# Performance work log

Hardware: AMD Instinct MI355X
Metric: run time of the kernel (lower is better)

The kernel has to match this reference:

```python
import jax, jax.numpy as jnp
import numpy as np

B, S, D = 4, 1024, 1024
H = 16
HD = D // H  # 64
NPOS = 64


def setup_inputs() -> dict:
    key = jax.random.key(0)
    ks = jax.random.split(key, 12)
    f = lambda k, shape, s=0.02: jax.random.normal(k, shape, dtype=jnp.float32) * s
    return {
        "q": jax.random.normal(ks[0], (B, S, D), dtype=jnp.float32),
        "k": jax.random.normal(ks[1], (B, S, D), dtype=jnp.float32),
        "v": jax.random.normal(ks[2], (B, S, D), dtype=jnp.float32),
        "Wq_w": f(ks[3], (D, D)), "Wq_b": f(ks[4], (D,)),
        "Wk_w": f(ks[5], (D, D)), "Wk_b": f(ks[6], (D,)),
        "Wv_w": f(ks[7], (D, D)), "Wv_b": f(ks[8], (D,)),
        "Wo_w": f(ks[9], (D, D)), "Wo_b": f(ks[10], (D,)),
        "pos_emb": f(ks[11], (HD, NPOS)),  # torch param is [1,1,head_dim,npos_max]
    }


def _proj(x, w, b):
    # nn.Linear: x @ w.T + b, then split heads -> [B, H, S, HD]
    y = jnp.einsum("bsd,ed->bse", x, w) + b
    bsz, s, _ = y.shape
    return y.reshape(bsz, s, H, HD).transpose(0, 2, 1, 3)


def reference(q, k, v, Wq_w, Wq_b, Wk_w, Wk_b, Wv_w, Wv_b, Wo_w, Wo_b, pos_emb):
    Q = _proj(q, Wq_w, Wq_b)
    K = _proj(k, Wk_w, Wk_b)
    V = _proj(v, Wv_w, Wv_b)

    scale = 1.0 / np.sqrt(HD).astype(np.float32)
    logits = jnp.einsum("bhqd,bhkd->bhqk", Q, K) * scale  # [B,H,S,S]

    # CoPE: sigmoid gates -> reverse cumsum -> interpolated position-logit gather
    gates = jax.nn.sigmoid(logits)
    pos = jnp.flip(jnp.cumsum(jnp.flip(gates, axis=-1), axis=-1), axis=-1)
    pos = jnp.minimum(pos, NPOS - 1)
    pos_floor = jnp.floor(pos)
    pos_ceil = jnp.ceil(pos)
    logits_int = jnp.einsum("bhqd,dn->bhqn", Q, pos_emb)  # [B,H,S,NPOS]
    lc = jnp.take_along_axis(logits_int, pos_ceil.astype(jnp.int32), axis=-1)
    lf = jnp.take_along_axis(logits_int, pos_floor.astype(jnp.int32), axis=-1)
    w = pos - pos_floor
    logits = logits + lc * w + lf * (1.0 - w)

    score = jax.nn.softmax(logits, axis=-1)
    out = jnp.einsum("bhqk,bhkd->bhqd", score, V)
    out = out.transpose(0, 2, 1, 3).reshape(q.shape[0], q.shape[1], D)
    return jnp.einsum("bsd,ed->bse", out, Wo_w) + Wo_b
```

## Files before the change

### kernel.cpp

```cpp
#include <hip/hip_runtime.h>
#include <hip/hip_bf16.h>

typedef __attribute__((ext_vector_type(8))) short short8;
typedef __attribute__((ext_vector_type(4))) float f32x4;
typedef unsigned short us;

#define MFMA16(a,b,c) __builtin_amdgcn_mfma_f32_16x16x32_bf16((a),(b),(c),0,0,0)
#define LOG2E 1.4426950408889634f

static __device__ __forceinline__ us bf16r(float x){
  unsigned u = __builtin_bit_cast(unsigned, x);
  u = u + 0x7fffu + ((u >> 16) & 1u);
  return (us)(u >> 16);
}
static __device__ __forceinline__ unsigned cvtpk(float a, float b){
  unsigned r; asm("v_cvt_pk_bf16_f32 %0, %1, %2" : "=v"(r) : "v"(a), "v"(b)); return r;
}
static __device__ __forceinline__ short8 cvt8(float4 a, float4 b){
  uint4 u; u.x = cvtpk(a.x, a.y); u.y = cvtpk(a.z, a.w);
  u.z = cvtpk(b.x, b.y); u.w = cvtpk(b.z, b.w);
  return __builtin_bit_cast(short8, u);
}
static __device__ __forceinline__ float b2f(us h){
  return __builtin_bit_cast(float, (unsigned)h << 16);
}
static __device__ __forceinline__ float exp2fast(float x){
  float r; asm("v_exp_f32 %0, %1" : "=v"(r) : "v"(x)); return r;
}
static __device__ __forceinline__ float rcpfast(float x){
  float r; asm("v_rcp_f32 %0, %1" : "=v"(r) : "v"(x)); return r;
}
static __device__ __forceinline__ float fractfast(float x){
  float r; asm("v_fract_f32 %0, %1" : "=v"(r) : "v"(x)); return r;
}
template<int CTRL, int RMASK>
static __device__ __forceinline__ float dpp_add(float x){
  int t = __builtin_amdgcn_update_dpp(0, __builtin_bit_cast(int, x), CTRL, RMASK, 0xf, false);
  return x + __builtin_bit_cast(float, t);
}
static __device__ __forceinline__ float wave_iscan(float x){
  x = dpp_add<0x111, 0xf>(x);
  x = dpp_add<0x112, 0xf>(x);
  x = dpp_add<0x114, 0xf>(x);
  x = dpp_add<0x118, 0xf>(x);
  x = dpp_add<0x142, 0xa>(x);
  x = dpp_add<0x143, 0xc>(x);
  return x;
}
static __device__ __forceinline__ float lane63(float x){
  return __builtin_bit_cast(float, __builtin_amdgcn_readlane(__builtin_bit_cast(int, x), 63));
}

__global__ __launch_bounds__(256)
void transpose_pe(const float* __restrict__ pe, us* __restrict__ peT){
  const int t = threadIdx.x;
  const int n = t & 63, dq = t >> 6;
#pragma unroll
  for (int j = 0; j < 16; ++j){
    const int d = dq * 16 + j;
    peT[n * 64 + d] = bf16r(pe[d * 64 + n] * LOG2E);
  }
}

__global__ __launch_bounds__(256)
void transpose_v(const us* __restrict__ Vb, us* __restrict__ VT){
  __shared__ __align__(16) us tile[64 * 72];
  const int t = threadIdx.x;
  const int stile = blockIdx.x & 15;
  const int bh = blockIdx.x >> 4;
  const int b = bh >> 4, h = bh & 15;
  const int s0 = stile << 6;
#pragma unroll
  for (int c = 0; c < 2; ++c){
    const int idx = t + (c << 8);
    const int sr = idx >> 3, cw = idx & 7;
    *(short8*)&tile[sr * 72 + cw * 8] =
        *(const short8*)(Vb + ((size_t)(b * 1024 + s0 + sr)) * 1024 + h * 64 + cw * 8);
  }
  __syncthreads();
#pragma unroll
  for (int c = 0; c < 2; ++c){
    const int idx = t + (c << 8);
    const int dr = idx >> 3, sw = idx & 7;
    short8 o;
#pragma unroll
    for (int j = 0; j < 8; ++j) o[j] = (short)tile[(sw * 8 + j) * 72 + dr];
    *(short8*)(VT + ((size_t)(bh * 64 + dr)) * 1024 + s0 + sw * 8) = o;
  }
}

template<bool A_BF16, bool OUT_BF16>
__global__ __launch_bounds__(256)
void gemm3(const void* __restrict__ Av0, const void* __restrict__ Av1, const void* __restrict__ Av2,
           const float* __restrict__ W0, const float* __restrict__ W1, const float* __restrict__ W2,
           const float* __restrict__ bp0, const float* __restrict__ bp1, const float* __restrict__ bp2,
           void* __restrict__ O0, void* __restrict__ O1, void* __restrict__ O2){
  __shared__ __align__(16) us Al[128 * 64];
  __shared__ __align__(16) us Bl[128 * 64];
  const int sel = blockIdx.y;
  const void* Av   = sel == 0 ? Av0 : (sel == 1 ? Av1 : Av2);
  const float* Wm  = sel == 0 ? W0  : (sel == 1 ? W1  : W2);
  const float* bias = sel == 0 ? bp0 : (sel == 1 ? bp1 : bp2);
  void* Ov         = sel == 0 ? O0  : (sel == 1 ? O1  : O2);
  const int tid = threadIdx.x;
  const int bm = blockIdx.x & 31, bn = blockIdx.x >> 5;
  const int m0 = bm << 7, n0 = bn << 7;
  const int w = tid >> 6, l = tid & 63;
  const int lr = l & 15, lg = l >> 4;
  const int wm = (w & 1) << 6, wn = (w >> 1) << 6;
  int srow[4], scol[4], sdst[4];
#pragma unroll
  for (int c = 0; c < 4; ++c){
    const int idx = tid + (c << 8);
    const int r = idx >> 3, cw = idx & 7;
    srow[c] = r; scol[c] = cw << 3;
    sdst[c] = r * 64 + ((cw << 3) ^ ((r & 7) << 3));
  }
  const int swz = (lr & 7) << 3;
  f32x4 acc[4][4];
#pragma unroll
  for (int i = 0; i < 4; ++i)
#pragma unroll
    for (int j = 0; j < 4; ++j) acc[i][j] = (f32x4){0.f, 0.f, 0.f, 0.f};

  auto ldA = [&](int c, int k) -> short8 {
    if constexpr (A_BF16){
      return *(const short8*)((const us*)Av + (size_t)(m0 + srow[c]) * 1024 + k + scol[c]);
    } else {
      const float* p = (const float*)Av + (size_t)(m0 + srow[c]) * 1024 + k + scol[c];
      return cvt8(*(const float4*)p, *(const float4*)(p + 4));
    }
  };
  auto ldW = [&](int c, int k) -> short8 {
    const float* p = Wm + (size_t)(n0 + srow[c]) * 1024 + k + scol[c];
    return cvt8(*(const float4*)p, *(const float4*)(p + 4));
  };

  short8 av[4], bv[4];
#pragma unroll
  for (int c = 0; c < 4; ++c){ av[c] = ldA(c, 0); bv[c] = ldW(c, 0); }

  for (int k0 = 0; k0 < 1024; k0 += 64){
    __syncthreads();
#pragma unroll
    for (int c = 0; c < 4; ++c){
      *(short8*)&Al[sdst[c]] = av[c];
      *(short8*)&Bl[sdst[c]] = bv[c];
    }
    __syncthreads();
    if (k0 < 960){
#pragma unroll
      for (int c = 0; c < 4; ++c){ av[c] = ldA(c, k0 + 64); bv[c] = ldW(c, k0 + 64); }
    }
#pragma unroll
    for (int ks = 0; ks < 2; ++ks){
      short8 af[4], bfv[4];
#pragma unroll
      for (int mt = 0; mt < 4; ++mt)
        af[mt] = *(const short8*)&Al[(wm + mt * 16 + lr) * 64 + (((ks << 5) + (lg << 3)) ^ swz)];
#pragma unroll
      for (int nt = 0; nt < 4; ++nt)
        bfv[nt] = *(const short8*)&Bl[(wn + nt * 16 + lr) * 64 + (((ks << 5) + (lg << 3)) ^ swz)];
#pragma unroll
      for (int mt = 0; mt < 4; ++mt)
#pragma unroll
        for (int nt = 0; nt < 4; ++nt)
          acc[mt][nt] = MFMA16(af[mt], bfv[nt], acc[mt][nt]);
    }
  }
  float bb[4];
#pragma unroll
  for (int nt = 0; nt < 4; ++nt) bb[nt] = bias[n0 + wn + nt * 16 + lr];
#pragma unroll
  for (int mt = 0; mt < 4; ++mt)
#pragma unroll
    for (int nt = 0; nt < 4; ++nt)
#pragma unroll
      for (int r = 0; r < 4; ++r){
        const size_t m = m0 + wm + mt * 16 + lg * 4 + r;
        const size_t n = n0 + wn + nt * 16 + lr;
        const float vv = acc[mt][nt][r] + bb[nt];
        if (OUT_BF16) ((us*)Ov)[m * 1024 + n] = bf16r(vv);
        else          ((float*)Ov)[m * 1024 + n] = vv;
      }
}

__global__ __launch_bounds__(256, 4)
void cope_attn_v13(const us* __restrict__ Qb, const us* __restrict__ Kb,
                   const us* __restrict__ VT, const us* __restrict__ peT,
                   us* __restrict__ Ob){
  __shared__ __align__(16) us yl[16 * 512];
  __shared__ float sums[16];
  const int tid = threadIdx.x;
  const int w = tid >> 6, l = tid & 63;
  const int lr = l & 15, lg = l >> 4;
  const int wg = ((blockIdx.x & 7) << 9) | (blockIdx.x >> 3);
  const int qt = wg & 63;
  const int bh = wg >> 6;
  const int b = bh >> 4, h = bh & 15;
  const int q0 = qt << 4;
  const us* Qh = Qb + ((size_t)(b * 1024 + q0)) * 1024 + h * 64;
  const us* Kh = Kb + ((size_t)(b * 1024)) * 1024 + h * 64;
  const us* Vh = VT + ((size_t)bh) * 64 * 1024;
  const float QSC = 0.125f * LOG2E;

  const short8 aq0 = *(const short8*)(Qh + (size_t)lr * 1024 + lg * 8);
  const short8 aq1 = *(const short8*)(Qh + (size_t)lr * 1024 + 32 + lg * 8);

  {
    f32x4 a = (f32x4){0.f, 0.f, 0.f, 0.f};
    const short8 p0 = *(const short8*)(peT + (size_t)(w * 16 + lr) * 64 + lg * 8);
    const short8 p1 = *(const short8*)(peT + (size_t)(w * 16 + lr) * 64 + 32 + lg * 8);
    a = MFMA16(aq0, p0, a);
    a = MFMA16(aq1, p1, a);
#pragma unroll
    for (int r = 0; r < 4; ++r) yl[(lg * 4 + r) * 64 + w * 16 + lr] = bf16r(a[r]);
  }
  __syncthreads();
  unsigned trow[4];
#pragma unroll
  for (int rr = 0; rr < 4; ++rr){
    const int row = w * 4 + rr;
    const us lov = yl[row * 64 + l];
    const us hiv = (l < 63) ? yl[row * 64 + l + 1] : lov;
    const float dif = b2f(hiv) - b2f(lov);
    trow[rr] = (unsigned)lov | ((unsigned)bf16r(dif) << 16);
  }

  float carry[4] = {0.f, 0.f, 0.f, 0.f};
  f32x4 oacc = (f32x4){0.f, 0.f, 0.f, 0.f};
  const int d0 = w * 16;
  const int psw = lr & 7;

  for (int c = 1; c >= 0; --c){
    const int koff = c << 9;
    __syncthreads();
    {
      const int kbase = w << 7;
      const us* Kw = Kh + (size_t)(koff + kbase + lr) * 1024 + lg * 8;
      for (int t = 0; t < 8; ++t){
        const short8 b0 = *(const short8*)(Kw + (size_t)(t * 16) * 1024);
        const short8 b1 = *(const short8*)(Kw + (size_t)(t * 16) * 1024 + 32);
        f32x4 a = (f32x4){0.f, 0.f, 0.f, 0.f};
        a = MFMA16(aq0, b0, a);
        a = MFMA16(aq1, b1, a);
        const int kc = kbase + t * 16 + lr;
        const unsigned p01 = cvtpk(a[0] * QSC, a[1] * QSC);
        const unsigned p23 = cvtpk(a[2] * QSC, a[3] * QSC);
        const int r0 = lg * 4;
        yl[(r0 + 0) * 512 + (((kc >> 3) ^ ((r0 + 0) & 7)) << 3) + (kc & 7)] = (us)p01;
        yl[(r0 + 1) * 512 + (((kc >> 3) ^ ((r0 + 1) & 7)) << 3) + (kc & 7)] = (us)(p01 >> 16);
        yl[(r0 + 2) * 512 + (((kc >> 3) ^ ((r0 + 2) & 7)) << 3) + (kc & 7)] = (us)p23;
        yl[(r0 + 3) * 512 + (((kc >> 3) ^ ((r0 + 3) & 7)) << 3) + (kc & 7)] = (us)(p23 >> 16);
      }
    }
    __syncthreads();
#pragma unroll
    for (int rr = 0; rr < 4; ++rr){
      const int row = w * 4 + rr;
      const int ad = row * 512 + ((l ^ (row & 7)) << 3);
      const short8 y0 = *(const short8*)&yl[ad];
      float x[8];
#pragma unroll
      for (int j = 0; j < 8; ++j) x[j] = b2f((us)y0[j]);
      float sum = 0.f;
      if (c == 0 && carry[rr] >= 63.f){
        const float li63 = b2f((us)(unsigned)__builtin_amdgcn_readlane((int)trow[rr], 63));
#pragma unroll
        for (int i = 0; i < 8; ++i){
          const float e = exp2fast(x[i] + li63);
          x[i] = e;
          sum += e;
        }
      } else {
        float g[8];
#pragma unroll
        for (int i = 0; i < 8; ++i) g[i] = rcpfast(1.f + exp2fast(-x[i]));
        const float a1 = g[0] + g[1];
        const float a3 = g[2] + g[3];
        const float a5 = g[4] + g[5];
        const float a7 = g[6] + g[7];
        const float b2v = g[2] + a1;
        const float b3v = a3 + a1;
        const float i4 = g[4] + b3v;
        const float i5 = a5 + b3v;
        const float i6 = g[6] + a5 + b3v;
        const float s  = a7 + a5 + b3v;
        float pref[8];
        pref[0] = 0.f;  pref[1] = g[0]; pref[2] = a1;  pref[3] = b2v;
        pref[4] = b3v;  pref[5] = i4;   pref[6] = i5;  pref[7] = i6;
        const float run = wave_iscan(s);
        const float T = lane63(run);
        const float base = carry[rr] + T - (run - s);
        carry[rr] += T;
        const unsigned tbl = trow[rr];
#pragma unroll
        for (int i = 0; i < 8; ++i){
          float p = base - pref[i];
          p = __builtin_amdgcn_fmed3f(p, 0.f, 63.f);
          const int il = (int)p;
          const float wt = fractfast(p);
          const unsigned pr = (unsigned)__builtin_amdgcn_ds_bpermute(il << 2, (int)tbl);
          const float lo  = __builtin_bit_cast(float, pr << 16);
          const float dif = __builtin_bit_cast(float, pr & 0xffff0000u);
          const float e = exp2fast(x[i] + lo + wt * dif);
          x[i] = e;
          sum += e;
        }
      }
      const float rs = lane63(wave_iscan(sum));
      if (l == 0){
        if (c == 1) sums[row] = rs;
        else        sums[row] += rs;
      }
      uint4 ua;
      ua.x = cvtpk(x[0], x[1]); ua.y = cvtpk(x[2], x[3]);
      ua.z = cvtpk(x[4], x[5]); ua.w = cvtpk(x[6], x[7]);
      *(uint4*)&yl[ad] = ua;
    }
    __syncthreads();
    {
      const us* Vw = Vh + (size_t)(d0 + lr) * 1024 + koff + lg * 8;
      for (int ks = 0; ks < 16; ++ks){
        const short8 vb = *(const short8*)(Vw + ks * 32);
        const short8 pa = *(const short8*)&yl[lr * 512 + ((((ks << 2) + lg) ^ psw) << 3)];
        oacc = MFMA16(pa, vb, oacc);
      }
    }
  }
  __syncthreads();
#pragma unroll
  for (int r = 0; r < 4; ++r){
    const float inv = rcpfast(sums[lg * 4 + r]);
    Ob[((size_t)(b * 1024 + q0 + lg * 4 + r)) * 1024 + h * 64 + d0 + lr] = bf16r(oacc[r] * inv);
  }
}

extern "C" void kernel_launch(void* const* d_in, const int* in_sizes, int n_in,
                              void* d_out, int out_size, void* d_ws, size_t ws_size,
                              hipStream_t stream) {
  const float* q    = (const float*)d_in[0];
  const float* k    = (const float*)d_in[1];
  const float* v    = (const float*)d_in[2];
  const float* Wq_w = (const float*)d_in[3];
  const float* Wq_b = (const float*)d_in[4];
  const float* Wk_w = (const float*)d_in[5];
  const float* Wk_b = (const float*)d_in[6];
  const float* Wv_w = (const float*)d_in[7];
  const float* Wv_b = (const float*)d_in[8];
  const float* Wo_w = (const float*)d_in[9];
  const float* Wo_b = (const float*)d_in[10];
  const float* pe   = (const float*)d_in[11];
  float* out = (float*)d_out;

  char* W = (char*)d_ws;
  const size_t MB = (size_t)1 << 20;
  us* Qbf = (us*)(W);
  us* Kbf = (us*)(W + 8 * MB);
  us* Vbf = (us*)(W + 16 * MB);
  us* VTb = (us*)(W + 24 * MB);
  us* Obf = (us*)(W + 32 * MB);
  us* peT = (us*)(W + 40 * MB);

  transpose_pe<<<1, 256, 0, stream>>>(pe, peT);
  gemm3<false, true><<<dim3(256, 3), 256, 0, stream>>>(
      q, k, v, Wq_w, Wk_w, Wv_w, Wq_b, Wk_b, Wv_b, Qbf, Kbf, Vbf);
  transpose_v<<<1024, 256, 0, stream>>>(Vbf, VTb);
  cope_attn_v13<<<4096, 256, 0, stream>>>(Qbf, Kbf, VTb, peT, Obf);
  gemm3<true, false><<<dim3(256, 1), 256, 0, stream>>>(
      Obf, Obf, Obf, Wo_w, Wo_w, Wo_w, Wo_b, Wo_b, Wo_b, out, out, out);
}
```

Baseline: 215.2 us.

## Fuse V transpose into projection GEMM epilogue and pack score rows in LDS

The V projection GEMM now writes its bf16 output directly in the transposed [b,h,d,s] layout from the epilogue, which removes the separate transpose_v kernel and its extra global round trip. Inside the attention kernel, the logit tile is stored as packed pairs of rows in 32-bit words. Each lane then reads two rows with one pair of vector loads and processes both rows from the same registers, replacing per-element 16-bit scattered LDS stores. The trade-off is strided 8-byte global stores in the GEMM epilogue and a more complex LDS addressing scheme.

```diff
diff --git a/kernel.cpp b/kernel.cpp
--- a/kernel.cpp
+++ b/kernel.cpp
@@ -23,6 +23,12 @@
 }
 static __device__ __forceinline__ float b2f(us h){
   return __builtin_bit_cast(float, (unsigned)h << 16);
+}
+static __device__ __forceinline__ float PKLO(unsigned u){
+  return __builtin_bit_cast(float, u << 16);
+}
+static __device__ __forceinline__ float PKHI(unsigned u){
+  return __builtin_bit_cast(float, u & 0xffff0000u);
 }
 static __device__ __forceinline__ float exp2fast(float x){
   float r; asm("v_exp_f32 %0, %1" : "=v"(r) : "v"(x)); return r;
@@ -62,39 +68,13 @@
   }
 }
 
-__global__ __launch_bounds__(256)
-void transpose_v(const us* __restrict__ Vb, us* __restrict__ VT){
-  __shared__ __align__(16) us tile[64 * 72];
-  const int t = threadIdx.x;
-  const int stile = blockIdx.x & 15;
-  const int bh = blockIdx.x >> 4;
-  const int b = bh >> 4, h = bh & 15;
-  const int s0 = stile << 6;
-#pragma unroll
-  for (int c = 0; c < 2; ++c){
-    const int idx = t + (c << 8);
-    const int sr = idx >> 3, cw = idx & 7;
-    *(short8*)&tile[sr * 72 + cw * 8] =
-        *(const short8*)(Vb + ((size_t)(b * 1024 + s0 + sr)) * 1024 + h * 64 + cw * 8);
-  }
-  __syncthreads();
-#pragma unroll
-  for (int c = 0; c < 2; ++c){
-    const int idx = t + (c << 8);
-    const int dr = idx >> 3, sw = idx & 7;
-    short8 o;
-#pragma unroll
-    for (int j = 0; j < 8; ++j) o[j] = (short)tile[(sw * 8 + j) * 72 + dr];
-    *(short8*)(VT + ((size_t)(bh * 64 + dr)) * 1024 + s0 + sw * 8) = o;
-  }
-}
-
 template<bool A_BF16, bool OUT_BF16>
 __global__ __launch_bounds__(256)
 void gemm3(const void* __restrict__ Av0, const void* __restrict__ Av1, const void* __restrict__ Av2,
            const float* __restrict__ W0, const float* __restrict__ W1, const float* __restrict__ W2,
            const float* __restrict__ bp0, const float* __restrict__ bp1, const float* __restrict__ bp2,
-           void* __restrict__ O0, void* __restrict__ O1, void* __restrict__ O2){
+           void* __restrict__ O0, void* __restrict__ O1, void* __restrict__ O2,
+           us* __restrict__ VTo){
   __shared__ __align__(16) us Al[128 * 64];
   __shared__ __align__(16) us Bl[128 * 64];
   const int sel = blockIdx.y;
@@ -171,6 +151,22 @@
   float bb[4];
 #pragma unroll
   for (int nt = 0; nt < 4; ++nt) bb[nt] = bias[n0 + wn + nt * 16 + lr];
+  if (VTo != nullptr && sel == 2){
+#pragma unroll
+    for (int mt = 0; mt < 4; ++mt)
+#pragma unroll
+      for (int nt = 0; nt < 4; ++nt){
+        const int n = n0 + wn + nt * 16 + lr;
+        const int hh = n >> 6, dd = n & 63;
+        const int mS = m0 + wm + mt * 16 + lg * 4;
+        const int bb2 = mS >> 10, ss = mS & 1023;
+        uint2 pk;
+        pk.x = cvtpk(acc[mt][nt][0] + bb[nt], acc[mt][nt][1] + bb[nt]);
+        pk.y = cvtpk(acc[mt][nt][2] + bb[nt], acc[mt][nt][3] + bb[nt]);
+        *(uint2*)&VTo[((size_t)((bb2 * 16 + hh) * 64 + dd)) * 1024 + ss] = pk;
+      }
+    return;
+  }
 #pragma unroll
   for (int mt = 0; mt < 4; ++mt)
 #pragma unroll
@@ -186,11 +182,13 @@
 }
 
 __global__ __launch_bounds__(256, 4)
-void cope_attn_v13(const us* __restrict__ Qb, const us* __restrict__ Kb,
+void cope_attn_v15(const us* __restrict__ Qb, const us* __restrict__ Kb,
                    const us* __restrict__ VT, const us* __restrict__ peT,
                    us* __restrict__ Ob){
-  __shared__ __align__(16) us yl[16 * 512];
+  __shared__ __align__(16) unsigned uls[8 * 512];
   __shared__ float sums[16];
+  us* yl16 = (us*)uls;
+  char* ybytes = (char*)uls;
   const int tid = threadIdx.x;
   const int w = tid >> 6, l = tid & 63;
   const int lr = l & 15, lg = l >> 4;
@@ -203,26 +201,27 @@
   const us* Kh = Kb + ((size_t)(b * 1024)) * 1024 + h * 64;
   const us* Vh = VT + ((size_t)bh) * 64 * 1024;
   const float QSC = 0.125f * LOG2E;
+  const f32x4 zf = (f32x4){0.f, 0.f, 0.f, 0.f};
 
   const short8 aq0 = *(const short8*)(Qh + (size_t)lr * 1024 + lg * 8);
   const short8 aq1 = *(const short8*)(Qh + (size_t)lr * 1024 + 32 + lg * 8);
 
   {
-    f32x4 a = (f32x4){0.f, 0.f, 0.f, 0.f};
+    f32x4 a = zf;
     const short8 p0 = *(const short8*)(peT + (size_t)(w * 16 + lr) * 64 + lg * 8);
     const short8 p1 = *(const short8*)(peT + (size_t)(w * 16 + lr) * 64 + 32 + lg * 8);
     a = MFMA16(aq0, p0, a);
     a = MFMA16(aq1, p1, a);
 #pragma unroll
-    for (int r = 0; r < 4; ++r) yl[(lg * 4 + r) * 64 + w * 16 + lr] = bf16r(a[r]);
+    for (int r = 0; r < 4; ++r) yl16[(lg * 4 + r) * 64 + w * 16 + lr] = bf16r(a[r]);
   }
   __syncthreads();
   unsigned trow[4];
 #pragma unroll
   for (int rr = 0; rr < 4; ++rr){
     const int row = w * 4 + rr;
-    const us lov = yl[row * 64 + l];
-    const us hiv = (l < 63) ? yl[row * 64 + l + 1] : lov;
+    const us lov = yl16[row * 64 + l];
+    const us hiv = (l < 63) ? yl16[row * 64 + l + 1] : lov;
     const float dif = b2f(hiv) - b2f(lov);
     trow[rr] = (unsigned)lov | ((unsigned)bf16r(dif) << 16);
   }
@@ -241,89 +240,94 @@
       for (int t = 0; t < 8; ++t){
         const short8 b0 = *(const short8*)(Kw + (size_t)(t * 16) * 1024);
         const short8 b1 = *(const short8*)(Kw + (size_t)(t * 16) * 1024 + 32);
-        f32x4 a = (f32x4){0.f, 0.f, 0.f, 0.f};
+        f32x4 a = zf;
         a = MFMA16(aq0, b0, a);
         a = MFMA16(aq1, b1, a);
         const int kc = kbase + t * 16 + lr;
-        const unsigned p01 = cvtpk(a[0] * QSC, a[1] * QSC);
-        const unsigned p23 = cvtpk(a[2] * QSC, a[3] * QSC);
-        const int r0 = lg * 4;
-        yl[(r0 + 0) * 512 + (((kc >> 3) ^ ((r0 + 0) & 7)) << 3) + (kc & 7)] = (us)p01;
-        yl[(r0 + 1) * 512 + (((kc >> 3) ^ ((r0 + 1) & 7)) << 3) + (kc & 7)] = (us)(p01 >> 16);
-        yl[(r0 + 2) * 512 + (((kc >> 3) ^ ((r0 + 2) & 7)) << 3) + (kc & 7)] = (us)p23;
-        yl[(r0 + 3) * 512 + (((kc >> 3) ^ ((r0 + 3) & 7)) << 3) + (kc & 7)] = (us)(p23 >> 16);
-      }
-    }
-    __syncthreads();
-#pragma unroll
-    for (int rr = 0; rr < 4; ++rr){
-      const int row = w * 4 + rr;
-      const int ad = row * 512 + ((l ^ (row & 7)) << 3);
-      const short8 y0 = *(const short8*)&yl[ad];
-      float x[8];
-#pragma unroll
-      for (int j = 0; j < 8; ++j) x[j] = b2f((us)y0[j]);
-      float sum = 0.f;
-      if (c == 0 && carry[rr] >= 63.f){
-        const float li63 = b2f((us)(unsigned)__builtin_amdgcn_readlane((int)trow[rr], 63));
-#pragma unroll
-        for (int i = 0; i < 8; ++i){
-          const float e = exp2fast(x[i] + li63);
-          x[i] = e;
-          sum += e;
+        uls[(lg * 2) * 512 + kc]     = cvtpk(a[0] * QSC, a[1] * QSC);
+        uls[(lg * 2 + 1) * 512 + kc] = cvtpk(a[2] * QSC, a[3] * QSC);
+      }
+    }
+    __syncthreads();
+#pragma unroll
+    for (int pp = 0; pp < 2; ++pp){
+      const int pr = w * 2 + pp;
+      const uint4 ra = *(const uint4*)&uls[pr * 512 + l * 8];
+      const uint4 rb = *(const uint4*)&uls[pr * 512 + l * 8 + 4];
+#pragma unroll
+      for (int par = 0; par < 2; ++par){
+        const int rr = pp * 2 + par;
+        const int row = w * 4 + rr;
+        float x[8];
+        if (par == 0){
+          x[0] = PKLO(ra.x); x[1] = PKLO(ra.y); x[2] = PKLO(ra.z); x[3] = PKLO(ra.w);
+          x[4] = PKLO(rb.x); x[5] = PKLO(rb.y); x[6] = PKLO(rb.z); x[7] = PKLO(rb.w);
+        } else {
+          x[0] = PKHI(ra.x); x[1] = PKHI(ra.y); x[2] = PKHI(ra.z); x[3] = PKHI(ra.w);
+          x[4] = PKHI(rb.x); x[5] = PKHI(rb.y); x[6] = PKHI(rb.z); x[7] = PKHI(rb.w);
         }
-      } else {
-        float g[8];
-#pragma unroll
-        for (int i = 0; i < 8; ++i) g[i] = rcpfast(1.f + exp2fast(-x[i]));
-        const float a1 = g[0] + g[1];
-        const float a3 = g[2] + g[3];
-        const float a5 = g[4] + g[5];
-        const float a7 = g[6] + g[7];
-        const float b2v = g[2] + a1;
-        const float b3v = a3 + a1;
-        const float i4 = g[4] + b3v;
-        const float i5 = a5 + b3v;
-        const float i6 = g[6] + a5 + b3v;
-        const float s  = a7 + a5 + b3v;
-        float pref[8];
-        pref[0] = 0.f;  pref[1] = g[0]; pref[2] = a1;  pref[3] = b2v;
-        pref[4] = b3v;  pref[5] = i4;   pref[6] = i5;  pref[7] = i6;
-        const float run = wave_iscan(s);
-        const float T = lane63(run);
-        const float base = carry[rr] + T - (run - s);
-        carry[rr] += T;
-        const unsigned tbl = trow[rr];
-#pragma unroll
-        for (int i = 0; i < 8; ++i){
-          float p = base - pref[i];
-          p = __builtin_amdgcn_fmed3f(p, 0.f, 63.f);
-          const int il = (int)p;
-          const float wt = fractfast(p);
-          const unsigned pr = (unsigned)__builtin_amdgcn_ds_bpermute(il << 2, (int)tbl);
-          const float lo  = __builtin_bit_cast(float, pr << 16);
-          const float dif = __builtin_bit_cast(float, pr & 0xffff0000u);
-          const float e = exp2fast(x[i] + lo + wt * dif);
-          x[i] = e;
-          sum += e;
+        float sum = 0.f;
+        if (c == 0 && carry[rr] >= 63.f){
+          const float li63 = b2f((us)(unsigned)__builtin_amdgcn_readlane((int)trow[rr], 63));
+#pragma unroll
+          for (int i = 0; i < 8; ++i){
+            const float e = exp2fast(x[i] + li63);
+            x[i] = e;
+            sum += e;
+          }
+        } else {
+          float g[8];
+#pragma unroll
+          for (int i = 0; i < 8; ++i) g[i] = rcpfast(1.f + exp2fast(-x[i]));
+          const float a1 = g[0] + g[1];
+          const float a3 = g[2] + g[3];
+          const float a5 = g[4] + g[5];
+          const float a7 = g[6] + g[7];
+          const float b2v = g[2] + a1;
+          const float b3v = a3 + a1;
+          const float i4 = g[4] + b3v;
+          const float i5 = a5 + b3v;
+          const float i6 = g[6] + a5 + b3v;
+          const float s  = a7 + a5 + b3v;
+          float pref[8];
+          pref[0] = 0.f;  pref[1] = g[0]; pref[2] = a1;  pref[3] = b2v;
+          pref[4] = b3v;  pref[5] = i4;   pref[6] = i5;  pref[7] = i6;
+          const float run = wave_iscan(s);
+          const float T = lane63(run);
+          const float base = carry[rr] + T - (run - s);
+          carry[rr] += T;
+          const unsigned tbl = trow[rr];
+#pragma unroll
+          for (int i = 0; i < 8; ++i){
+            float p = base - pref[i];
+            p = __builtin_amdgcn_fmed3f(p, 0.f, 63.f);
+            const int il = (int)p;
+            const float wt = fractfast(p);
+            const unsigned pr2 = (unsigned)__builtin_amdgcn_ds_bpermute(il << 2, (int)tbl);
+            const float lo  = __builtin_bit_cast(float, pr2 << 16);
+            const float dif = __builtin_bit_cast(float, pr2 & 0xffff0000u);
+            const float e = exp2fast(x[i] + lo + wt * dif);
+            x[i] = e;
+            sum += e;
+          }
         }
-      }
-      const float rs = lane63(wave_iscan(sum));
-      if (l == 0){
-        if (c == 1) sums[row] = rs;
-        else        sums[row] += rs;
-      }
-      uint4 ua;
-      ua.x = cvtpk(x[0], x[1]); ua.y = cvtpk(x[2], x[3]);
-      ua.z = cvtpk(x[4], x[5]); ua.w = cvtpk(x[6], x[7]);
-      *(uint4*)&yl[ad] = ua;
+        const float rs = lane63(wave_iscan(sum));
+        if (l == 0){
+          if (c == 1) sums[row] = rs;
+          else        sums[row] += rs;
+        }
+        uint4 ua;
+        ua.x = cvtpk(x[0], x[1]); ua.y = cvtpk(x[2], x[3]);
+        ua.z = cvtpk(x[4], x[5]); ua.w = cvtpk(x[6], x[7]);
+        *(uint4*)(ybytes + row * 1024 + ((l ^ (row & 7)) << 4)) = ua;
+      }
     }
     __syncthreads();
     {
       const us* Vw = Vh + (size_t)(d0 + lr) * 1024 + koff + lg * 8;
       for (int ks = 0; ks < 16; ++ks){
         const short8 vb = *(const short8*)(Vw + ks * 32);
-        const short8 pa = *(const short8*)&yl[lr * 512 + ((((ks << 2) + lg) ^ psw) << 3)];
+        const short8 pa = *(const short8*)(ybytes + lr * 1024 + ((((ks << 2) + lg) ^ psw) << 4));
         oacc = MFMA16(pa, vb, oacc);
       }
     }
@@ -364,9 +368,8 @@
 
   transpose_pe<<<1, 256, 0, stream>>>(pe, peT);
   gemm3<false, true><<<dim3(256, 3), 256, 0, stream>>>(
-      q, k, v, Wq_w, Wk_w, Wv_w, Wq_b, Wk_b, Wv_b, Qbf, Kbf, Vbf);
-  transpose_v<<<1024, 256, 0, stream>>>(Vbf, VTb);
-  cope_attn_v13<<<4096, 256, 0, stream>>>(Qbf, Kbf, VTb, peT, Obf);
+      q, k, v, Wq_w, Wk_w, Wv_w, Wq_b, Wk_b, Wv_b, Qbf, Kbf, Vbf, VTb);
+  cope_attn_v15<<<4096, 256, 0, stream>>>(Qbf, Kbf, VTb, peT, Obf);
   gemm3<true, false><<<dim3(256, 1), 256, 0, stream>>>(
-      Obf, Obf, Obf, Wo_w, Wo_w, Wo_w, Wo_b, Wo_b, Wo_b, out, out, out);
-}
+      Obf, Obf, Obf, Wo_w, Wo_w, Wo_w, Wo_b, Wo_b, Wo_b, out, out, out, nullptr);
+}
```

Measured after the change: 213.9 us. Within noise of the previous version (-0.6%).
